# Kernel optimization log

Hardware: AMD Instinct MI355X
Metric: run time of the kernel (lower is better)

## Reference

```python
import jax, jax.numpy as jnp
import numpy as np

FEATURE_DIM = 4
LOSS_WEIGHT = 1.0
DELTA_V = 0.5
DELTA_D = 1.5
NUM_LABELS = 8  # instance ids 0..7; 0 = background
B, H, W = 16, 640, 640


def _safe_norm(x, axis):
    # L2 norm with grad-safe sqrt (forward value exact: 0 when sum of squares is 0)
    sq = jnp.sum(x * x, axis=axis)
    pos = sq > 0
    return jnp.where(pos, jnp.sqrt(jnp.where(pos, sq, 1.0)), 0.0)


def _single_loss(emb, instance, kernel, training_mask):
    # emb: [H,W,C], instance: [H,W] int, kernel/training_mask: [H,W] float
    C = emb.shape[-1]
    L = NUM_LABELS
    tm = training_mask > 0.5
    kr = kernel > 0.5
    inst = jnp.where(tm, instance, 0).reshape(-1)          # [P]
    inst_k = jnp.where(kr.reshape(-1), inst, 0)            # [P]
    emb_f = emb.reshape(-1, C)                              # [P,C]

    # per-label kernel-region means (emb_mean), label 0 column is zeros
    sums = jax.ops.segment_sum(emb_f, inst_k, num_segments=L)                       # [L,C]
    cnts = jax.ops.segment_sum(jnp.ones(inst_k.shape, jnp.float32), inst_k, L)      # [L]
    mu = sums / jnp.maximum(cnts, 1.0)[:, None]
    mu = mu.at[0].set(0.0)

    # aggregation term: per-pixel distance to its instance mean
    d = _safe_norm(emb_f - mu[inst], axis=1)                                         # [P]
    term = jnp.log(jnp.maximum(d - DELTA_V, 0.0) ** 2 + 1.0)
    cnt_i = jax.ops.segment_sum(jnp.ones(inst.shape, jnp.float32), inst, L)
    agg = jax.ops.segment_sum(term, inst, L) / jnp.maximum(cnt_i, 1.0)               # [L]
    # original skips label 0, then takes mean of l_agg[1:] -> drops first nonzero label
    l_agg = jnp.mean(agg[2:])

    # discrimination term: all ordered pairs of distinct nonzero labels
    dd = _safe_norm(mu[:, None, :] - mu[None, :, :], axis=-1)                        # [L,L]
    valid = (1.0 - jnp.eye(L, dtype=jnp.float32)).at[0, :].set(0.0).at[:, 0].set(0.0)
    dis = jnp.log(jnp.maximum(2.0 * DELTA_D - dd, 0.0) ** 2 + 1.0)
    l_dis = jnp.sum(dis * valid) / jnp.sum(valid)

    l_reg = jnp.mean(jnp.log(_safe_norm(mu, axis=1) + 1.0)) * 0.001
    return l_agg + l_dis + l_reg


def reference(emb, instance, kernel, training_mask):
    losses = jax.vmap(_single_loss)(emb, instance, kernel, training_mask)  # [B]
    return LOSS_WEIGHT * jnp.mean(losses)


def setup_inputs() -> dict:
    key = jax.random.key(0)
    k1, k2, k3 = jax.random.split(key, 3)
    emb = jax.random.normal(k1, (B, H, W, FEATURE_DIM), dtype=jnp.float32)
    instance = jax.random.randint(k2, (B, H, W), 0, NUM_LABELS, dtype=jnp.int32)
    kernel = jax.random.uniform(k3, (B, H, W), dtype=jnp.float32)
    training_mask = jnp.ones((B, H, W), dtype=jnp.float32)
    return {"emb": emb, "instance": instance, "kernel": kernel, "training_mask": training_mask}
```

## Files before the change

kernel.cpp:

```cpp
#include <hip/hip_runtime.h>
#include <math.h>

#define NLAB 8
#define BATCH 16
#define S_OFF  0
#define CK_OFF 28
#define CI_OFF 35
#define AG_OFF 41
#define ACC_PER_B 48
#define CNT_IDX (BATCH * ACC_PER_B)
#define ACC_ZERO_BYTES ((CNT_IDX + 1) * 4)
#define LAB_OFFSET 4096
#define GRID_X 64

__device__ __forceinline__ float wave_reduce(float v) {
#pragma unroll
  for (int off = 32; off > 0; off >>= 1) v += __shfl_xor(v, off, 64);
  return v;
}

__global__ __launch_bounds__(256, 4) void k_accum(
    const float4* __restrict__ emb, const int* __restrict__ inst,
    const float* __restrict__ ker, const float* __restrict__ tmk,
    float* __restrict__ acc, unsigned char* __restrict__ labc,
    int P, int use_cache)
{
  const int b = blockIdx.y;
  const size_t base = (size_t)b * P;
  const float4* e  = emb + base;
  const int*    ip = inst + base;
  const float*  kp = ker + base;
  const float*  tp = tmk + base;
  unsigned char* lb = labc + base;

  float s[28];
#pragma unroll
  for (int k = 0; k < 28; ++k) s[k] = 0.f;
  int ck[7] = {0, 0, 0, 0, 0, 0, 0};
  int ci[6] = {0, 0, 0, 0, 0, 0};

  const int lane = threadIdx.x & 63;
  const int wid  = threadIdx.x >> 6;
  const int ntiles = P >> 10;

  for (int t = blockIdx.x; t < ntiles; t += gridDim.x) {
    const int p0 = (t << 10) + (wid << 8) + lane;
    float4 e0 = e[p0];
    float4 e1 = e[p0 + 64];
    float4 e2 = e[p0 + 128];
    float4 e3 = e[p0 + 192];
    int   v0 = ip[p0], v1 = ip[p0 + 64], v2 = ip[p0 + 128], v3 = ip[p0 + 192];
    float q0 = kp[p0], q1 = kp[p0 + 64], q2 = kp[p0 + 128], q3 = kp[p0 + 192];
    float u0 = tp[p0], u1 = tp[p0 + 64], u2 = tp[p0 + 128], u3 = tp[p0 + 192];

    int lab0 = (u0 > 0.5f) ? (v0 & 7) : 0;
    int lab1 = (u1 > 0.5f) ? (v1 & 7) : 0;
    int lab2 = (u2 > 0.5f) ? (v2 & 7) : 0;
    int lab3 = (u3 > 0.5f) ? (v3 & 7) : 0;
    if (use_cache) {
      lb[p0]       = (unsigned char)lab0;
      lb[p0 + 64]  = (unsigned char)lab1;
      lb[p0 + 128] = (unsigned char)lab2;
      lb[p0 + 192] = (unsigned char)lab3;
    }
    int lk0 = (q0 > 0.5f) ? lab0 : 8;
    int lk1 = (q1 > 0.5f) ? lab1 : 8;
    int lk2 = (q2 > 0.5f) ? lab2 : 8;
    int lk3 = (q3 > 0.5f) ? lab3 : 8;

#pragma unroll
    for (int l = 1; l < NLAB; ++l) {
      bool h0 = (lk0 == l), h1 = (lk1 == l), h2 = (lk2 == l), h3 = (lk3 == l);
      ck[l - 1] += __popcll(__ballot(h0)) + __popcll(__ballot(h1)) +
                   __popcll(__ballot(h2)) + __popcll(__ballot(h3));
      float m0 = h0 ? 1.f : 0.f, m1 = h1 ? 1.f : 0.f;
      float m2 = h2 ? 1.f : 0.f, m3 = h3 ? 1.f : 0.f;
      const int o = (l - 1) * 4;
      s[o + 0] = fmaf(m0, e0.x, fmaf(m1, e1.x, fmaf(m2, e2.x, fmaf(m3, e3.x, s[o + 0]))));
      s[o + 1] = fmaf(m0, e0.y, fmaf(m1, e1.y, fmaf(m2, e2.y, fmaf(m3, e3.y, s[o + 1]))));
      s[o + 2] = fmaf(m0, e0.z, fmaf(m1, e1.z, fmaf(m2, e2.z, fmaf(m3, e3.z, s[o + 2]))));
      s[o + 3] = fmaf(m0, e0.w, fmaf(m1, e1.w, fmaf(m2, e2.w, fmaf(m3, e3.w, s[o + 3]))));
    }
#pragma unroll
    for (int l = 2; l < NLAB; ++l) {
      ci[l - 2] += __popcll(__ballot(lab0 == l)) + __popcll(__ballot(lab1 == l)) +
                   __popcll(__ballot(lab2 == l)) + __popcll(__ballot(lab3 == l));
    }
  }

  if (blockIdx.x == 0) {
    for (int p = (ntiles << 10) + (int)threadIdx.x; p < P; p += (int)blockDim.x) {
      int lab = (tp[p] > 0.5f) ? (ip[p] & 7) : 0;
      float kr = kp[p];
      float4 ev = e[p];
      if (lab >= 1 && kr > 0.5f) {
        atomicAdd(&acc[b * ACC_PER_B + (lab - 1) * 4 + 0], ev.x);
        atomicAdd(&acc[b * ACC_PER_B + (lab - 1) * 4 + 1], ev.y);
        atomicAdd(&acc[b * ACC_PER_B + (lab - 1) * 4 + 2], ev.z);
        atomicAdd(&acc[b * ACC_PER_B + (lab - 1) * 4 + 3], ev.w);
        atomicAdd(&acc[b * ACC_PER_B + CK_OFF + lab - 1], 1.f);
      }
      if (lab >= 2) atomicAdd(&acc[b * ACC_PER_B + CI_OFF + lab - 2], 1.f);
    }
  }

#pragma unroll
  for (int off = 32; off > 0; off >>= 1) {
    float tsh[28];
#pragma unroll
    for (int k = 0; k < 28; ++k) tsh[k] = __shfl_xor(s[k], off, 64);
#pragma unroll
    for (int k = 0; k < 28; ++k) s[k] += tsh[k];
  }

  __shared__ float redf[4][28];
  __shared__ int   redi[4][13];
  if (lane == 0) {
#pragma unroll
    for (int k = 0; k < 28; ++k) redf[wid][k] = s[k];
#pragma unroll
    for (int k = 0; k < 7; ++k) redi[wid][k] = ck[k];
#pragma unroll
    for (int k = 0; k < 6; ++k) redi[wid][7 + k] = ci[k];
  }
  __syncthreads();
  if (threadIdx.x < 28) {
    float v = redf[0][threadIdx.x] + redf[1][threadIdx.x] +
              redf[2][threadIdx.x] + redf[3][threadIdx.x];
    atomicAdd(acc + b * ACC_PER_B + S_OFF + threadIdx.x, v);
  } else if (threadIdx.x >= 32 && threadIdx.x < 32 + 13) {
    int j = threadIdx.x - 32;
    int v = redi[0][j] + redi[1][j] + redi[2][j] + redi[3][j];
    atomicAdd(acc + b * ACC_PER_B + CK_OFF + j, (float)v);
  }
}

__global__ __launch_bounds__(256, 4) void k_agg(
    const float4* __restrict__ emb, const int* __restrict__ inst,
    const float* __restrict__ tmk, const unsigned char* __restrict__ labc,
    float* __restrict__ acc, float* __restrict__ out,
    int P, int use_cache, int nblocks)
{
  const int b = blockIdx.y;
  const size_t base = (size_t)b * P;
  __shared__ float4 smu[NLAB];
  const float* accB = acc + b * ACC_PER_B;
  if (threadIdx.x < NLAB) {
    int l = threadIdx.x;
    float4 m = make_float4(0.f, 0.f, 0.f, 0.f);
    if (l > 0) {
      float inv = 1.f / fmaxf(accB[CK_OFF + l - 1], 1.f);
      m = make_float4(accB[S_OFF + (l - 1) * 4 + 0] * inv,
                      accB[S_OFF + (l - 1) * 4 + 1] * inv,
                      accB[S_OFF + (l - 1) * 4 + 2] * inv,
                      accB[S_OFF + (l - 1) * 4 + 3] * inv);
    }
    smu[l] = m;
  }
  __syncthreads();

  const float4* e = emb + base;
  const int*    ip = inst + base;
  const float*  tp = tmk + base;
  const unsigned char* lb = labc + base;

  float ag[6] = {0.f, 0.f, 0.f, 0.f, 0.f, 0.f};
  const int lane = threadIdx.x & 63;
  const int wid  = threadIdx.x >> 6;
  const int ntiles = P >> 10;

  for (int t = blockIdx.x; t < ntiles; t += gridDim.x) {
    const int p0 = (t << 10) + (wid << 8) + lane;
    int lab0, lab1, lab2, lab3;
    if (use_cache) {
      lab0 = lb[p0]; lab1 = lb[p0 + 64]; lab2 = lb[p0 + 128]; lab3 = lb[p0 + 192];
    } else {
      lab0 = (tp[p0] > 0.5f)       ? (ip[p0] & 7)       : 0;
      lab1 = (tp[p0 + 64] > 0.5f)  ? (ip[p0 + 64] & 7)  : 0;
      lab2 = (tp[p0 + 128] > 0.5f) ? (ip[p0 + 128] & 7) : 0;
      lab3 = (tp[p0 + 192] > 0.5f) ? (ip[p0 + 192] & 7) : 0;
    }
    float4 e0 = e[p0];
    float4 e1 = e[p0 + 64];
    float4 e2 = e[p0 + 128];
    float4 e3 = e[p0 + 192];

#pragma unroll
    for (int i = 0; i < 4; ++i) {
      int lab = (i == 0) ? lab0 : (i == 1) ? lab1 : (i == 2) ? lab2 : lab3;
      float4 ev = (i == 0) ? e0 : (i == 1) ? e1 : (i == 2) ? e2 : e3;
      float4 mv = smu[lab];
      float dx = ev.x - mv.x, dy = ev.y - mv.y;
      float dz = ev.z - mv.z, dw = ev.w - mv.w;
      float sq = dx * dx + dy * dy + dz * dz + dw * dw;
      float d = sqrtf(sq);
      float tt = fmaxf(d - 0.5f, 0.f);
      float term = logf(fmaf(tt, tt, 1.f));
#pragma unroll
      for (int l = 0; l < 6; ++l) ag[l] += (lab == l + 2) ? term : 0.f;
    }
  }

  if (blockIdx.x == 0) {
    for (int p = (ntiles << 10) + (int)threadIdx.x; p < P; p += (int)blockDim.x) {
      int lab = (tp[p] > 0.5f) ? (ip[p] & 7) : 0;
      if (lab >= 2) {
        float4 ev = e[p]; float4 mv = smu[lab];
        float dx = ev.x - mv.x, dy = ev.y - mv.y;
        float dz = ev.z - mv.z, dw = ev.w - mv.w;
        float d = sqrtf(dx * dx + dy * dy + dz * dz + dw * dw);
        float tt = fmaxf(d - 0.5f, 0.f);
        atomicAdd(&acc[b * ACC_PER_B + AG_OFF + lab - 2], logf(fmaf(tt, tt, 1.f)));
      }
    }
  }

#pragma unroll
  for (int off = 32; off > 0; off >>= 1) {
    float tsh[6];
#pragma unroll
    for (int k = 0; k < 6; ++k) tsh[k] = __shfl_xor(ag[k], off, 64);
#pragma unroll
    for (int k = 0; k < 6; ++k) ag[k] += tsh[k];
  }
  __shared__ float redf[4][6];
  if (lane == 0) {
#pragma unroll
    for (int k = 0; k < 6; ++k) redf[wid][k] = ag[k];
  }
  __syncthreads();
  if (threadIdx.x < 6) {
    float v = redf[0][threadIdx.x] + redf[1][threadIdx.x] +
              redf[2][threadIdx.x] + redf[3][threadIdx.x];
    atomicAdd(acc + b * ACC_PER_B + AG_OFF + threadIdx.x, v);
  }

  __syncthreads();
  __shared__ int amlast;
  if (threadIdx.x == 0) {
    __threadfence();
    unsigned int* cnt = (unsigned int*)(acc + CNT_IDX);
    unsigned int old = atomicAdd(cnt, 1u);
    amlast = (old == (unsigned int)(nblocks - 1)) ? 1 : 0;
  }
  __syncthreads();
  if (amlast && threadIdx.x < 64) {
    __threadfence();
    float loss = 0.f;
    if (threadIdx.x < BATCH) {
      const float* a = acc + threadIdx.x * ACC_PER_B;
      float av[47];
#pragma unroll
      for (int k = 0; k < 47; ++k)
        av[k] = __hip_atomic_load(&a[k], __ATOMIC_RELAXED, __HIP_MEMORY_SCOPE_AGENT);
      float mu[NLAB][4];
#pragma unroll
      for (int c = 0; c < 4; ++c) mu[0][c] = 0.f;
#pragma unroll
      for (int l = 1; l < NLAB; ++l) {
        float inv = 1.f / fmaxf(av[CK_OFF + l - 1], 1.f);
#pragma unroll
        for (int c = 0; c < 4; ++c) mu[l][c] = av[S_OFF + (l - 1) * 4 + c] * inv;
      }
      float l_agg = 0.f;
#pragma unroll
      for (int l = 2; l < NLAB; ++l)
        l_agg += av[AG_OFF + l - 2] / fmaxf(av[CI_OFF + l - 2], 1.f);
      l_agg *= (1.f / 6.f);
      float ssum = 0.f;
      for (int i = 1; i < NLAB; ++i)
        for (int j = 1; j < NLAB; ++j) {
          if (i == j) continue;
          float dx = mu[i][0] - mu[j][0], dy = mu[i][1] - mu[j][1];
          float dz = mu[i][2] - mu[j][2], dw = mu[i][3] - mu[j][3];
          float dd = sqrtf(dx * dx + dy * dy + dz * dz + dw * dw);
          float tt = fmaxf(3.0f - dd, 0.f);
          ssum += logf(fmaf(tt, tt, 1.f));
        }
      float l_dis = ssum / 42.f;
      float rsum = 0.f;
#pragma unroll
      for (int l = 1; l < NLAB; ++l) {
        float n = sqrtf(mu[l][0] * mu[l][0] + mu[l][1] * mu[l][1] +
                        mu[l][2] * mu[l][2] + mu[l][3] * mu[l][3]);
        rsum += logf(n + 1.f);
      }
      float l_reg = rsum * (0.001f / NLAB);
      loss = l_agg + l_dis + l_reg;
    }
    loss = wave_reduce(loss);
    if (threadIdx.x == 0) out[0] = loss * (1.f / BATCH);
  }
}

extern "C" void kernel_launch(void* const* d_in, const int* in_sizes, int n_in,
                              void* d_out, int out_size, void* d_ws, size_t ws_size,
                              hipStream_t stream) {
  const float4* emb  = (const float4*)d_in[0];
  const int*    inst = (const int*)d_in[1];
  const float*  ker  = (const float*)d_in[2];
  const float*  tmk  = (const float*)d_in[3];
  float* out = (float*)d_out;

  const int total = in_sizes[1];
  const int P = total / BATCH;

  float* acc = (float*)d_ws;
  unsigned char* labc = (unsigned char*)d_ws + LAB_OFFSET;
  const size_t need = (size_t)LAB_OFFSET + (size_t)total;
  const int use_cache = (ws_size >= need) ? 1 : 0;

  hipMemsetAsync(d_ws, 0, ACC_ZERO_BYTES, stream);

  dim3 grid(GRID_X, BATCH);
  k_accum<<<grid, 256, 0, stream>>>(emb, inst, ker, tmk, acc, labc, P, use_cache);
  k_agg  <<<grid, 256, 0, stream>>>(emb, inst, tmk, labc, acc, out, P, use_cache,
                                    GRID_X * BATCH);
}
```

Measured before the change: 272.3 us.

## Fuse accumulate and aggregate passes into one kernel with a grid barrier

```diff
diff --git a/kernel.cpp b/kernel.cpp
--- a/kernel.cpp
+++ b/kernel.cpp
@@ -8,10 +8,11 @@
 #define CI_OFF 35
 #define AG_OFF 41
 #define ACC_PER_B 48
-#define CNT_IDX (BATCH * ACC_PER_B)
-#define ACC_ZERO_BYTES ((CNT_IDX + 1) * 4)
-#define LAB_OFFSET 4096
-#define GRID_X 64
+#define CNT1_IDX (BATCH * ACC_PER_B)
+#define CNT2_IDX (BATCH * ACC_PER_B + 1)
+#define ACC_ZERO_BYTES ((BATCH * ACC_PER_B + 2) * 4)
+#define GX 64
+#define MAXK 8
 
 __device__ __forceinline__ float wave_reduce(float v) {
 #pragma unroll
@@ -19,19 +20,30 @@
   return v;
 }
 
-__global__ __launch_bounds__(256, 4) void k_accum(
+__global__ __launch_bounds__(256, 4) void k_fused(
     const float4* __restrict__ emb, const int* __restrict__ inst,
     const float* __restrict__ ker, const float* __restrict__ tmk,
-    float* __restrict__ acc, unsigned char* __restrict__ labc,
-    int P, int use_cache)
+    float* __restrict__ acc, float* __restrict__ out,
+    int P, int nblocks)
 {
+  __shared__ unsigned char labL[MAXK * 1024];
+  __shared__ float redf[4][28];
+  __shared__ int   redi[4][13];
+  __shared__ float accL[ACC_PER_B];
+  __shared__ float4 smu_s[NLAB];
+  __shared__ float redg[4][6];
+
   const int b = blockIdx.y;
   const size_t base = (size_t)b * P;
   const float4* e  = emb + base;
   const int*    ip = inst + base;
   const float*  kp = ker + base;
   const float*  tp = tmk + base;
-  unsigned char* lb = labc + base;
+
+  const int lane = threadIdx.x & 63;
+  const int wid  = threadIdx.x >> 6;
+  const int ntiles = P >> 10;
+  const int tail = P - (ntiles << 10);
 
   float s[28];
 #pragma unroll
@@ -39,56 +51,56 @@
   int ck[7] = {0, 0, 0, 0, 0, 0, 0};
   int ci[6] = {0, 0, 0, 0, 0, 0};
 
-  const int lane = threadIdx.x & 63;
-  const int wid  = threadIdx.x >> 6;
-  const int ntiles = P >> 10;
-
-  for (int t = blockIdx.x; t < ntiles; t += gridDim.x) {
-    const int p0 = (t << 10) + (wid << 8) + lane;
-    float4 e0 = e[p0];
-    float4 e1 = e[p0 + 64];
-    float4 e2 = e[p0 + 128];
-    float4 e3 = e[p0 + 192];
-    int   v0 = ip[p0], v1 = ip[p0 + 64], v2 = ip[p0 + 128], v3 = ip[p0 + 192];
-    float q0 = kp[p0], q1 = kp[p0 + 64], q2 = kp[p0 + 128], q3 = kp[p0 + 192];
-    float u0 = tp[p0], u1 = tp[p0 + 64], u2 = tp[p0 + 128], u3 = tp[p0 + 192];
-
-    int lab0 = (u0 > 0.5f) ? (v0 & 7) : 0;
-    int lab1 = (u1 > 0.5f) ? (v1 & 7) : 0;
-    int lab2 = (u2 > 0.5f) ? (v2 & 7) : 0;
-    int lab3 = (u3 > 0.5f) ? (v3 & 7) : 0;
-    if (use_cache) {
-      lb[p0]       = (unsigned char)lab0;
-      lb[p0 + 64]  = (unsigned char)lab1;
-      lb[p0 + 128] = (unsigned char)lab2;
-      lb[p0 + 192] = (unsigned char)lab3;
-    }
-    int lk0 = (q0 > 0.5f) ? lab0 : 8;
-    int lk1 = (q1 > 0.5f) ? lab1 : 8;
-    int lk2 = (q2 > 0.5f) ? lab2 : 8;
-    int lk3 = (q3 > 0.5f) ? lab3 : 8;
-
-#pragma unroll
-    for (int l = 1; l < NLAB; ++l) {
-      bool h0 = (lk0 == l), h1 = (lk1 == l), h2 = (lk2 == l), h3 = (lk3 == l);
-      ck[l - 1] += __popcll(__ballot(h0)) + __popcll(__ballot(h1)) +
-                   __popcll(__ballot(h2)) + __popcll(__ballot(h3));
-      float m0 = h0 ? 1.f : 0.f, m1 = h1 ? 1.f : 0.f;
-      float m2 = h2 ? 1.f : 0.f, m3 = h3 ? 1.f : 0.f;
-      const int o = (l - 1) * 4;
-      s[o + 0] = fmaf(m0, e0.x, fmaf(m1, e1.x, fmaf(m2, e2.x, fmaf(m3, e3.x, s[o + 0]))));
-      s[o + 1] = fmaf(m0, e0.y, fmaf(m1, e1.y, fmaf(m2, e2.y, fmaf(m3, e3.y, s[o + 1]))));
-      s[o + 2] = fmaf(m0, e0.z, fmaf(m1, e1.z, fmaf(m2, e2.z, fmaf(m3, e3.z, s[o + 2]))));
-      s[o + 3] = fmaf(m0, e0.w, fmaf(m1, e1.w, fmaf(m2, e2.w, fmaf(m3, e3.w, s[o + 3]))));
-    }
-#pragma unroll
-    for (int l = 2; l < NLAB; ++l) {
-      ci[l - 2] += __popcll(__ballot(lab0 == l)) + __popcll(__ballot(lab1 == l)) +
-                   __popcll(__ballot(lab2 == l)) + __popcll(__ballot(lab3 == l));
-    }
-  }
-
-  if (blockIdx.x == 0) {
+  {
+    int k = 0;
+    for (int t = blockIdx.x; t < ntiles; t += GX, ++k) {
+      const int p0 = (t << 10) + (wid << 8) + lane;
+      float4 e0 = e[p0];
+      float4 e1 = e[p0 + 64];
+      float4 e2 = e[p0 + 128];
+      float4 e3 = e[p0 + 192];
+      int   v0 = ip[p0], v1 = ip[p0 + 64], v2 = ip[p0 + 128], v3 = ip[p0 + 192];
+      float q0 = kp[p0], q1 = kp[p0 + 64], q2 = kp[p0 + 128], q3 = kp[p0 + 192];
+      float u0 = tp[p0], u1 = tp[p0 + 64], u2 = tp[p0 + 128], u3 = tp[p0 + 192];
+
+      int lab0 = (u0 > 0.5f) ? (v0 & 7) : 0;
+      int lab1 = (u1 > 0.5f) ? (v1 & 7) : 0;
+      int lab2 = (u2 > 0.5f) ? (v2 & 7) : 0;
+      int lab3 = (u3 > 0.5f) ? (v3 & 7) : 0;
+      if (k < MAXK) {
+        const int lo = (k << 10) + (wid << 8) + lane;
+        labL[lo]       = (unsigned char)lab0;
+        labL[lo + 64]  = (unsigned char)lab1;
+        labL[lo + 128] = (unsigned char)lab2;
+        labL[lo + 192] = (unsigned char)lab3;
+      }
+      int lk0 = (q0 > 0.5f) ? lab0 : 8;
+      int lk1 = (q1 > 0.5f) ? lab1 : 8;
+      int lk2 = (q2 > 0.5f) ? lab2 : 8;
+      int lk3 = (q3 > 0.5f) ? lab3 : 8;
+
+#pragma unroll
+      for (int l = 1; l < NLAB; ++l) {
+        bool h0 = (lk0 == l), h1 = (lk1 == l), h2 = (lk2 == l), h3 = (lk3 == l);
+        ck[l - 1] += __popcll(__ballot(h0)) + __popcll(__ballot(h1)) +
+                     __popcll(__ballot(h2)) + __popcll(__ballot(h3));
+        float m0 = h0 ? 1.f : 0.f, m1 = h1 ? 1.f : 0.f;
+        float m2 = h2 ? 1.f : 0.f, m3 = h3 ? 1.f : 0.f;
+        const int o = (l - 1) * 4;
+        s[o + 0] = fmaf(m0, e0.x, fmaf(m1, e1.x, fmaf(m2, e2.x, fmaf(m3, e3.x, s[o + 0]))));
+        s[o + 1] = fmaf(m0, e0.y, fmaf(m1, e1.y, fmaf(m2, e2.y, fmaf(m3, e3.y, s[o + 1]))));
+        s[o + 2] = fmaf(m0, e0.z, fmaf(m1, e1.z, fmaf(m2, e2.z, fmaf(m3, e3.z, s[o + 2]))));
+        s[o + 3] = fmaf(m0, e0.w, fmaf(m1, e1.w, fmaf(m2, e2.w, fmaf(m3, e3.w, s[o + 3]))));
+      }
+#pragma unroll
+      for (int l = 2; l < NLAB; ++l) {
+        ci[l - 2] += __popcll(__ballot(lab0 == l)) + __popcll(__ballot(lab1 == l)) +
+                     __popcll(__ballot(lab2 == l)) + __popcll(__ballot(lab3 == l));
+      }
+    }
+  }
+
+  if (tail && blockIdx.x == 0) {
     for (int p = (ntiles << 10) + (int)threadIdx.x; p < P; p += (int)blockDim.x) {
       int lab = (tp[p] > 0.5f) ? (ip[p] & 7) : 0;
       float kr = kp[p];
@@ -102,6 +114,7 @@
       }
       if (lab >= 2) atomicAdd(&acc[b * ACC_PER_B + CI_OFF + lab - 2], 1.f);
     }
+    __threadfence();
   }
 
 #pragma unroll
@@ -112,9 +125,6 @@
 #pragma unroll
     for (int k = 0; k < 28; ++k) s[k] += tsh[k];
   }
-
-  __shared__ float redf[4][28];
-  __shared__ int   redi[4][13];
   if (lane == 0) {
 #pragma unroll
     for (int k = 0; k < 28; ++k) redf[wid][k] = s[k];
@@ -133,75 +143,75 @@
     int v = redi[0][j] + redi[1][j] + redi[2][j] + redi[3][j];
     atomicAdd(acc + b * ACC_PER_B + CK_OFF + j, (float)v);
   }
-}
-
-__global__ __launch_bounds__(256, 4) void k_agg(
-    const float4* __restrict__ emb, const int* __restrict__ inst,
-    const float* __restrict__ tmk, const unsigned char* __restrict__ labc,
-    float* __restrict__ acc, float* __restrict__ out,
-    int P, int use_cache, int nblocks)
-{
-  const int b = blockIdx.y;
-  const size_t base = (size_t)b * P;
-  __shared__ float4 smu[NLAB];
-  const float* accB = acc + b * ACC_PER_B;
+
+  if (threadIdx.x == 0) {
+    unsigned int* cnt = (unsigned int*)(acc + CNT1_IDX);
+    __hip_atomic_fetch_add(cnt, 1u, __ATOMIC_ACQ_REL, __HIP_MEMORY_SCOPE_AGENT);
+    while (__hip_atomic_load(cnt, __ATOMIC_ACQUIRE, __HIP_MEMORY_SCOPE_AGENT)
+           < (unsigned int)nblocks)
+      __builtin_amdgcn_s_sleep(2);
+  }
+  __syncthreads();
+
+  if (threadIdx.x < 47)
+    accL[threadIdx.x] = __hip_atomic_load(&acc[b * ACC_PER_B + threadIdx.x],
+                                          __ATOMIC_RELAXED, __HIP_MEMORY_SCOPE_AGENT);
+  __syncthreads();
   if (threadIdx.x < NLAB) {
     int l = threadIdx.x;
     float4 m = make_float4(0.f, 0.f, 0.f, 0.f);
     if (l > 0) {
-      float inv = 1.f / fmaxf(accB[CK_OFF + l - 1], 1.f);
-      m = make_float4(accB[S_OFF + (l - 1) * 4 + 0] * inv,
-                      accB[S_OFF + (l - 1) * 4 + 1] * inv,
-                      accB[S_OFF + (l - 1) * 4 + 2] * inv,
-                      accB[S_OFF + (l - 1) * 4 + 3] * inv);
-    }
-    smu[l] = m;
-  }
-  __syncthreads();
-
-  const float4* e = emb + base;
-  const int*    ip = inst + base;
-  const float*  tp = tmk + base;
-  const unsigned char* lb = labc + base;
+      float inv = 1.f / fmaxf(accL[CK_OFF + l - 1], 1.f);
+      m = make_float4(accL[S_OFF + (l - 1) * 4 + 0] * inv,
+                      accL[S_OFF + (l - 1) * 4 + 1] * inv,
+                      accL[S_OFF + (l - 1) * 4 + 2] * inv,
+                      accL[S_OFF + (l - 1) * 4 + 3] * inv);
+    }
+    smu_s[l] = m;
+  }
+  __syncthreads();
+  float4 smu[NLAB];
+#pragma unroll
+  for (int l = 0; l < NLAB; ++l) smu[l] = smu_s[l];
 
   float ag[6] = {0.f, 0.f, 0.f, 0.f, 0.f, 0.f};
-  const int lane = threadIdx.x & 63;
-  const int wid  = threadIdx.x >> 6;
-  const int ntiles = P >> 10;
-
-  for (int t = blockIdx.x; t < ntiles; t += gridDim.x) {
-    const int p0 = (t << 10) + (wid << 8) + lane;
-    int lab0, lab1, lab2, lab3;
-    if (use_cache) {
-      lab0 = lb[p0]; lab1 = lb[p0 + 64]; lab2 = lb[p0 + 128]; lab3 = lb[p0 + 192];
-    } else {
-      lab0 = (tp[p0] > 0.5f)       ? (ip[p0] & 7)       : 0;
-      lab1 = (tp[p0 + 64] > 0.5f)  ? (ip[p0 + 64] & 7)  : 0;
-      lab2 = (tp[p0 + 128] > 0.5f) ? (ip[p0 + 128] & 7) : 0;
-      lab3 = (tp[p0 + 192] > 0.5f) ? (ip[p0 + 192] & 7) : 0;
-    }
-    float4 e0 = e[p0];
-    float4 e1 = e[p0 + 64];
-    float4 e2 = e[p0 + 128];
-    float4 e3 = e[p0 + 192];
-
-#pragma unroll
-    for (int i = 0; i < 4; ++i) {
-      int lab = (i == 0) ? lab0 : (i == 1) ? lab1 : (i == 2) ? lab2 : lab3;
-      float4 ev = (i == 0) ? e0 : (i == 1) ? e1 : (i == 2) ? e2 : e3;
-      float4 mv = smu[lab];
-      float dx = ev.x - mv.x, dy = ev.y - mv.y;
-      float dz = ev.z - mv.z, dw = ev.w - mv.w;
-      float sq = dx * dx + dy * dy + dz * dz + dw * dw;
-      float d = sqrtf(sq);
-      float tt = fmaxf(d - 0.5f, 0.f);
-      float term = logf(fmaf(tt, tt, 1.f));
-#pragma unroll
-      for (int l = 0; l < 6; ++l) ag[l] += (lab == l + 2) ? term : 0.f;
-    }
-  }
-
-  if (blockIdx.x == 0) {
+  {
+    int k = 0;
+    for (int t = blockIdx.x; t < ntiles; t += GX, ++k) {
+      const int p0 = (t << 10) + (wid << 8) + lane;
+      int lab0, lab1, lab2, lab3;
+      if (k < MAXK) {
+        const int lo = (k << 10) + (wid << 8) + lane;
+        lab0 = labL[lo]; lab1 = labL[lo + 64];
+        lab2 = labL[lo + 128]; lab3 = labL[lo + 192];
+      } else {
+        lab0 = (tp[p0] > 0.5f)       ? (ip[p0] & 7)       : 0;
+        lab1 = (tp[p0 + 64] > 0.5f)  ? (ip[p0 + 64] & 7)  : 0;
+        lab2 = (tp[p0 + 128] > 0.5f) ? (ip[p0 + 128] & 7) : 0;
+        lab3 = (tp[p0 + 192] > 0.5f) ? (ip[p0 + 192] & 7) : 0;
+      }
+      float4 e0 = e[p0];
+      float4 e1 = e[p0 + 64];
+      float4 e2 = e[p0 + 128];
+      float4 e3 = e[p0 + 192];
+
+#pragma unroll
+      for (int i = 0; i < 4; ++i) {
+        int lab = (i == 0) ? lab0 : (i == 1) ? lab1 : (i == 2) ? lab2 : lab3;
+        float4 ev = (i == 0) ? e0 : (i == 1) ? e1 : (i == 2) ? e2 : e3;
+        float4 mv = smu[lab];
+        float dx = ev.x - mv.x, dy = ev.y - mv.y;
+        float dz = ev.z - mv.z, dw = ev.w - mv.w;
+        float d = sqrtf(dx * dx + dy * dy + dz * dz + dw * dw);
+        float tt = fmaxf(d - 0.5f, 0.f);
+        float term = logf(fmaf(tt, tt, 1.f));
+#pragma unroll
+        for (int l = 0; l < 6; ++l) ag[l] += (lab == l + 2) ? term : 0.f;
+      }
+    }
+  }
+
+  if (tail && blockIdx.x == 0) {
     for (int p = (ntiles << 10) + (int)threadIdx.x; p < P; p += (int)blockDim.x) {
       int lab = (tp[p] > 0.5f) ? (ip[p] & 7) : 0;
       if (lab >= 2) {
@@ -213,6 +223,7 @@
         atomicAdd(&acc[b * ACC_PER_B + AG_OFF + lab - 2], logf(fmaf(tt, tt, 1.f)));
       }
     }
+    __threadfence();
   }
 
 #pragma unroll
@@ -223,29 +234,27 @@
 #pragma unroll
     for (int k = 0; k < 6; ++k) ag[k] += tsh[k];
   }
-  __shared__ float redf[4][6];
   if (lane == 0) {
 #pragma unroll
-    for (int k = 0; k < 6; ++k) redf[wid][k] = ag[k];
+    for (int k = 0; k < 6; ++k) redg[wid][k] = ag[k];
   }
   __syncthreads();
   if (threadIdx.x < 6) {
-    float v = redf[0][threadIdx.x] + redf[1][threadIdx.x] +
-              redf[2][threadIdx.x] + redf[3][threadIdx.x];
+    float v = redg[0][threadIdx.x] + redg[1][threadIdx.x] +
+              redg[2][threadIdx.x] + redg[3][threadIdx.x];
     atomicAdd(acc + b * ACC_PER_B + AG_OFF + threadIdx.x, v);
   }
 
   __syncthreads();
   __shared__ int amlast;
   if (threadIdx.x == 0) {
-    __threadfence();
-    unsigned int* cnt = (unsigned int*)(acc + CNT_IDX);
-    unsigned int old = atomicAdd(cnt, 1u);
+    unsigned int* cnt = (unsigned int*)(acc + CNT2_IDX);
+    unsigned int old = __hip_atomic_fetch_add(cnt, 1u, __ATOMIC_ACQ_REL,
+                                              __HIP_MEMORY_SCOPE_AGENT);
     amlast = (old == (unsigned int)(nblocks - 1)) ? 1 : 0;
   }
   __syncthreads();
   if (amlast && threadIdx.x < 64) {
-    __threadfence();
     float loss = 0.f;
     if (threadIdx.x < BATCH) {
       const float* a = acc + threadIdx.x * ACC_PER_B;
@@ -306,14 +315,9 @@
   const int P = total / BATCH;
 
   float* acc = (float*)d_ws;
-  unsigned char* labc = (unsigned char*)d_ws + LAB_OFFSET;
-  const size_t need = (size_t)LAB_OFFSET + (size_t)total;
-  const int use_cache = (ws_size >= need) ? 1 : 0;
 
   hipMemsetAsync(d_ws, 0, ACC_ZERO_BYTES, stream);
 
-  dim3 grid(GRID_X, BATCH);
-  k_accum<<<grid, 256, 0, stream>>>(emb, inst, ker, tmk, acc, labc, P, use_cache);
-  k_agg  <<<grid, 256, 0, stream>>>(emb, inst, tmk, labc, acc, out, P, use_cache,
-                                    GRID_X * BATCH);
+  dim3 grid(GX, BATCH);
+  k_fused<<<grid, 256, 0, stream>>>(emb, inst, ker, tmk, acc, out, P, GX * BATCH);
 }
```

Measured after the change: 444.5 us. 63.2% more time.

## Process 16 contiguous pixels per thread with vectorized loads and packed label cache

Applied to the files above, without the earlier changes.

```diff
diff --git a/kernel.cpp b/kernel.cpp
--- a/kernel.cpp
+++ b/kernel.cpp
@@ -11,7 +11,11 @@
 #define CNT_IDX (BATCH * ACC_PER_B)
 #define ACC_ZERO_BYTES ((CNT_IDX + 1) * 4)
 #define LAB_OFFSET 4096
-#define GRID_X 64
+#define GX 64
+
+#define GETI(v, c) ((c) == 0 ? (v).x : (c) == 1 ? (v).y : (c) == 2 ? (v).z : (v).w)
+#define GETF(v, c) ((c) == 0 ? (v).x : (c) == 1 ? (v).y : (c) == 2 ? (v).z : (v).w)
+#define GETU(v, c) ((c) == 0 ? (v).x : (c) == 1 ? (v).y : (c) == 2 ? (v).z : (v).w)
 
 __device__ __forceinline__ float wave_reduce(float v) {
 #pragma unroll
@@ -19,11 +23,11 @@
   return v;
 }
 
-__global__ __launch_bounds__(256, 4) void k_accum(
+__global__ __launch_bounds__(256, 2) void k_accum(
     const float4* __restrict__ emb, const int* __restrict__ inst,
     const float* __restrict__ ker, const float* __restrict__ tmk,
     float* __restrict__ acc, unsigned char* __restrict__ labc,
-    int P, int use_cache)
+    int P, int use_cache, int fast)
 {
   const int b = blockIdx.y;
   const size_t base = (size_t)b * P;
@@ -39,60 +43,74 @@
   int ck[7] = {0, 0, 0, 0, 0, 0, 0};
   int ci[6] = {0, 0, 0, 0, 0, 0};
 
-  const int lane = threadIdx.x & 63;
-  const int wid  = threadIdx.x >> 6;
-  const int ntiles = P >> 10;
-
-  for (int t = blockIdx.x; t < ntiles; t += gridDim.x) {
-    const int p0 = (t << 10) + (wid << 8) + lane;
-    float4 e0 = e[p0];
-    float4 e1 = e[p0 + 64];
-    float4 e2 = e[p0 + 128];
-    float4 e3 = e[p0 + 192];
-    int   v0 = ip[p0], v1 = ip[p0 + 64], v2 = ip[p0 + 128], v3 = ip[p0 + 192];
-    float q0 = kp[p0], q1 = kp[p0 + 64], q2 = kp[p0 + 128], q3 = kp[p0 + 192];
-    float u0 = tp[p0], u1 = tp[p0 + 64], u2 = tp[p0 + 128], u3 = tp[p0 + 192];
-
-    int lab0 = (u0 > 0.5f) ? (v0 & 7) : 0;
-    int lab1 = (u1 > 0.5f) ? (v1 & 7) : 0;
-    int lab2 = (u2 > 0.5f) ? (v2 & 7) : 0;
-    int lab3 = (u3 > 0.5f) ? (v3 & 7) : 0;
-    if (use_cache) {
-      lb[p0]       = (unsigned char)lab0;
-      lb[p0 + 64]  = (unsigned char)lab1;
-      lb[p0 + 128] = (unsigned char)lab2;
-      lb[p0 + 192] = (unsigned char)lab3;
-    }
-    int lk0 = (q0 > 0.5f) ? lab0 : 8;
-    int lk1 = (q1 > 0.5f) ? lab1 : 8;
-    int lk2 = (q2 > 0.5f) ? lab2 : 8;
-    int lk3 = (q3 > 0.5f) ? lab3 : 8;
-
-#pragma unroll
-    for (int l = 1; l < NLAB; ++l) {
-      bool h0 = (lk0 == l), h1 = (lk1 == l), h2 = (lk2 == l), h3 = (lk3 == l);
-      ck[l - 1] += __popcll(__ballot(h0)) + __popcll(__ballot(h1)) +
-                   __popcll(__ballot(h2)) + __popcll(__ballot(h3));
-      float m0 = h0 ? 1.f : 0.f, m1 = h1 ? 1.f : 0.f;
-      float m2 = h2 ? 1.f : 0.f, m3 = h3 ? 1.f : 0.f;
-      const int o = (l - 1) * 4;
-      s[o + 0] = fmaf(m0, e0.x, fmaf(m1, e1.x, fmaf(m2, e2.x, fmaf(m3, e3.x, s[o + 0]))));
-      s[o + 1] = fmaf(m0, e0.y, fmaf(m1, e1.y, fmaf(m2, e2.y, fmaf(m3, e3.y, s[o + 1]))));
-      s[o + 2] = fmaf(m0, e0.z, fmaf(m1, e1.z, fmaf(m2, e2.z, fmaf(m3, e3.z, s[o + 2]))));
-      s[o + 3] = fmaf(m0, e0.w, fmaf(m1, e1.w, fmaf(m2, e2.w, fmaf(m3, e3.w, s[o + 3]))));
-    }
-#pragma unroll
-    for (int l = 2; l < NLAB; ++l) {
-      ci[l - 2] += __popcll(__ballot(lab0 == l)) + __popcll(__ballot(lab1 == l)) +
-                   __popcll(__ballot(lab2 == l)) + __popcll(__ballot(lab3 == l));
-    }
-  }
-
-  if (blockIdx.x == 0) {
-    for (int p = (ntiles << 10) + (int)threadIdx.x; p < P; p += (int)blockDim.x) {
+  const int tid = blockIdx.x * blockDim.x + threadIdx.x;
+  const int nthreads = gridDim.x * blockDim.x;
+
+  if (fast) {
+    const int nu = P >> 4;
+    const int4*   ip4 = (const int4*)ip;
+    const float4* kp4 = (const float4*)kp;
+    const float4* tp4 = (const float4*)tp;
+    uint4* lb4 = (uint4*)lb;
+
+    for (int u = tid; u < nu; u += nthreads) {
+      int4   iv[4]; float4 kv[4], tv[4]; float4 ev[16];
+#pragma unroll
+      for (int a = 0; a < 4; ++a) iv[a] = ip4[u * 4 + a];
+#pragma unroll
+      for (int a = 0; a < 4; ++a) kv[a] = kp4[u * 4 + a];
+#pragma unroll
+      for (int a = 0; a < 4; ++a) tv[a] = tp4[u * 4 + a];
+#pragma unroll
+      for (int j = 0; j < 16; ++j) ev[j] = e[u * 16 + j];
+
+      int lab[16], lk[16];
+#pragma unroll
+      for (int j = 0; j < 16; ++j) {
+        int   v = GETI(iv[j >> 2], j & 3);
+        float q = GETF(kv[j >> 2], j & 3);
+        float t = GETF(tv[j >> 2], j & 3);
+        lab[j] = (t > 0.5f) ? (v & 7) : 0;
+        lk[j]  = (q > 0.5f) ? lab[j] : 8;
+      }
+      if (use_cache) {
+        uint4 pk;
+        pk.x = (unsigned)lab[0]  | ((unsigned)lab[1]  << 8) | ((unsigned)lab[2]  << 16) | ((unsigned)lab[3]  << 24);
+        pk.y = (unsigned)lab[4]  | ((unsigned)lab[5]  << 8) | ((unsigned)lab[6]  << 16) | ((unsigned)lab[7]  << 24);
+        pk.z = (unsigned)lab[8]  | ((unsigned)lab[9]  << 8) | ((unsigned)lab[10] << 16) | ((unsigned)lab[11] << 24);
+        pk.w = (unsigned)lab[12] | ((unsigned)lab[13] << 8) | ((unsigned)lab[14] << 16) | ((unsigned)lab[15] << 24);
+        lb4[u] = pk;
+      }
+#pragma unroll
+      for (int l = 1; l < NLAB; ++l) {
+        int c = 0;
+        const int o = (l - 1) * 4;
+#pragma unroll
+        for (int j = 0; j < 16; ++j) {
+          bool h = (lk[j] == l);
+          c += __popcll(__ballot(h));
+          float m = h ? 1.f : 0.f;
+          s[o + 0] = fmaf(m, ev[j].x, s[o + 0]);
+          s[o + 1] = fmaf(m, ev[j].y, s[o + 1]);
+          s[o + 2] = fmaf(m, ev[j].z, s[o + 2]);
+          s[o + 3] = fmaf(m, ev[j].w, s[o + 3]);
+        }
+        ck[l - 1] += c;
+      }
+#pragma unroll
+      for (int l = 2; l < NLAB; ++l) {
+        int c = 0;
+#pragma unroll
+        for (int j = 0; j < 16; ++j) c += __popcll(__ballot(lab[j] == l));
+        ci[l - 2] += c;
+      }
+    }
+    const int p0 = nu << 4;
+    for (int p = p0 + tid; p < P; p += nthreads) {
       int lab = (tp[p] > 0.5f) ? (ip[p] & 7) : 0;
       float kr = kp[p];
       float4 ev = e[p];
+      if (use_cache) lb[p] = (unsigned char)lab;
       if (lab >= 1 && kr > 0.5f) {
         atomicAdd(&acc[b * ACC_PER_B + (lab - 1) * 4 + 0], ev.x);
         atomicAdd(&acc[b * ACC_PER_B + (lab - 1) * 4 + 1], ev.y);
@@ -102,8 +120,25 @@
       }
       if (lab >= 2) atomicAdd(&acc[b * ACC_PER_B + CI_OFF + lab - 2], 1.f);
     }
-  }
-
+  } else {
+    for (int p = tid; p < P; p += nthreads) {
+      int lab = (tp[p] > 0.5f) ? (ip[p] & 7) : 0;
+      float kr = kp[p];
+      float4 ev = e[p];
+      if (use_cache) lb[p] = (unsigned char)lab;
+      if (lab >= 1 && kr > 0.5f) {
+        atomicAdd(&acc[b * ACC_PER_B + (lab - 1) * 4 + 0], ev.x);
+        atomicAdd(&acc[b * ACC_PER_B + (lab - 1) * 4 + 1], ev.y);
+        atomicAdd(&acc[b * ACC_PER_B + (lab - 1) * 4 + 2], ev.z);
+        atomicAdd(&acc[b * ACC_PER_B + (lab - 1) * 4 + 3], ev.w);
+        atomicAdd(&acc[b * ACC_PER_B + CK_OFF + lab - 1], 1.f);
+      }
+      if (lab >= 2) atomicAdd(&acc[b * ACC_PER_B + CI_OFF + lab - 2], 1.f);
+    }
+  }
+
+  const int lane = threadIdx.x & 63;
+  const int wid  = threadIdx.x >> 6;
 #pragma unroll
   for (int off = 32; off > 0; off >>= 1) {
     float tsh[28];
@@ -112,7 +147,6 @@
 #pragma unroll
     for (int k = 0; k < 28; ++k) s[k] += tsh[k];
   }
-
   __shared__ float redf[4][28];
   __shared__ int   redi[4][13];
   if (lane == 0) {
@@ -135,15 +169,15 @@
   }
 }
 
-__global__ __launch_bounds__(256, 4) void k_agg(
+__global__ __launch_bounds__(256, 2) void k_agg(
     const float4* __restrict__ emb, const int* __restrict__ inst,
     const float* __restrict__ tmk, const unsigned char* __restrict__ labc,
     float* __restrict__ acc, float* __restrict__ out,
-    int P, int use_cache, int nblocks)
+    int P, int use_cache, int fast, int nblocks)
 {
   const int b = blockIdx.y;
   const size_t base = (size_t)b * P;
-  __shared__ float4 smu[NLAB];
+  __shared__ float4 smu_s[NLAB];
   const float* accB = acc + b * ACC_PER_B;
   if (threadIdx.x < NLAB) {
     int l = threadIdx.x;
@@ -155,54 +189,65 @@
                       accB[S_OFF + (l - 1) * 4 + 2] * inv,
                       accB[S_OFF + (l - 1) * 4 + 3] * inv);
     }
-    smu[l] = m;
-  }
-  __syncthreads();
-
-  const float4* e = emb + base;
+    smu_s[l] = m;
+  }
+  __syncthreads();
+  float4 smu[NLAB];
+#pragma unroll
+  for (int l = 0; l < NLAB; ++l) smu[l] = smu_s[l];
+
+  const float4* e  = emb + base;
   const int*    ip = inst + base;
   const float*  tp = tmk + base;
   const unsigned char* lb = labc + base;
 
   float ag[6] = {0.f, 0.f, 0.f, 0.f, 0.f, 0.f};
-  const int lane = threadIdx.x & 63;
-  const int wid  = threadIdx.x >> 6;
-  const int ntiles = P >> 10;
-
-  for (int t = blockIdx.x; t < ntiles; t += gridDim.x) {
-    const int p0 = (t << 10) + (wid << 8) + lane;
-    int lab0, lab1, lab2, lab3;
-    if (use_cache) {
-      lab0 = lb[p0]; lab1 = lb[p0 + 64]; lab2 = lb[p0 + 128]; lab3 = lb[p0 + 192];
-    } else {
-      lab0 = (tp[p0] > 0.5f)       ? (ip[p0] & 7)       : 0;
-      lab1 = (tp[p0 + 64] > 0.5f)  ? (ip[p0 + 64] & 7)  : 0;
-      lab2 = (tp[p0 + 128] > 0.5f) ? (ip[p0 + 128] & 7) : 0;
-      lab3 = (tp[p0 + 192] > 0.5f) ? (ip[p0 + 192] & 7) : 0;
-    }
-    float4 e0 = e[p0];
-    float4 e1 = e[p0 + 64];
-    float4 e2 = e[p0 + 128];
-    float4 e3 = e[p0 + 192];
-
-#pragma unroll
-    for (int i = 0; i < 4; ++i) {
-      int lab = (i == 0) ? lab0 : (i == 1) ? lab1 : (i == 2) ? lab2 : lab3;
-      float4 ev = (i == 0) ? e0 : (i == 1) ? e1 : (i == 2) ? e2 : e3;
-      float4 mv = smu[lab];
-      float dx = ev.x - mv.x, dy = ev.y - mv.y;
-      float dz = ev.z - mv.z, dw = ev.w - mv.w;
-      float sq = dx * dx + dy * dy + dz * dz + dw * dw;
-      float d = sqrtf(sq);
-      float tt = fmaxf(d - 0.5f, 0.f);
-      float term = logf(fmaf(tt, tt, 1.f));
-#pragma unroll
-      for (int l = 0; l < 6; ++l) ag[l] += (lab == l + 2) ? term : 0.f;
-    }
-  }
-
-  if (blockIdx.x == 0) {
-    for (int p = (ntiles << 10) + (int)threadIdx.x; p < P; p += (int)blockDim.x) {
+  const int tid = blockIdx.x * blockDim.x + threadIdx.x;
+  const int nthreads = gridDim.x * blockDim.x;
+
+  if (fast) {
+    const int nu = P >> 4;
+    const uint4* lb4 = (const uint4*)lb;
+    const int4*   ip4 = (const int4*)ip;
+    const float4* tp4 = (const float4*)tp;
+
+    for (int u = tid; u < nu; u += nthreads) {
+      float4 ev[16];
+#pragma unroll
+      for (int j = 0; j < 16; ++j) ev[j] = e[u * 16 + j];
+      int lab[16];
+      if (use_cache) {
+        uint4 lq = lb4[u];
+#pragma unroll
+        for (int j = 0; j < 16; ++j)
+          lab[j] = (GETU(lq, j >> 2) >> ((j & 3) * 8)) & 7;
+      } else {
+        int4 iv[4]; float4 tv[4];
+#pragma unroll
+        for (int a = 0; a < 4; ++a) iv[a] = ip4[u * 4 + a];
+#pragma unroll
+        for (int a = 0; a < 4; ++a) tv[a] = tp4[u * 4 + a];
+#pragma unroll
+        for (int j = 0; j < 16; ++j) {
+          int   v = GETI(iv[j >> 2], j & 3);
+          float t = GETF(tv[j >> 2], j & 3);
+          lab[j] = (t > 0.5f) ? (v & 7) : 0;
+        }
+      }
+#pragma unroll
+      for (int j = 0; j < 16; ++j) {
+        float4 mv = smu[lab[j]];
+        float dx = ev[j].x - mv.x, dy = ev[j].y - mv.y;
+        float dz = ev[j].z - mv.z, dw = ev[j].w - mv.w;
+        float d = sqrtf(dx * dx + dy * dy + dz * dz + dw * dw);
+        float tt = fmaxf(d - 0.5f, 0.f);
+        float term = logf(fmaf(tt, tt, 1.f));
+#pragma unroll
+        for (int l = 0; l < 6; ++l) ag[l] += (lab[j] == l + 2) ? term : 0.f;
+      }
+    }
+    const int p0 = nu << 4;
+    for (int p = p0 + tid; p < P; p += nthreads) {
       int lab = (tp[p] > 0.5f) ? (ip[p] & 7) : 0;
       if (lab >= 2) {
         float4 ev = e[p]; float4 mv = smu[lab];
@@ -213,8 +258,22 @@
         atomicAdd(&acc[b * ACC_PER_B + AG_OFF + lab - 2], logf(fmaf(tt, tt, 1.f)));
       }
     }
-  }
-
+  } else {
+    for (int p = tid; p < P; p += nthreads) {
+      int lab = (tp[p] > 0.5f) ? (ip[p] & 7) : 0;
+      if (lab >= 2) {
+        float4 ev = e[p]; float4 mv = smu[lab];
+        float dx = ev.x - mv.x, dy = ev.y - mv.y;
+        float dz = ev.z - mv.z, dw = ev.w - mv.w;
+        float d = sqrtf(dx * dx + dy * dy + dz * dz + dw * dw);
+        float tt = fmaxf(d - 0.5f, 0.f);
+        atomicAdd(&acc[b * ACC_PER_B + AG_OFF + lab - 2], logf(fmaf(tt, tt, 1.f)));
+      }
+    }
+  }
+
+  const int lane = threadIdx.x & 63;
+  const int wid  = threadIdx.x >> 6;
 #pragma unroll
   for (int off = 32; off > 0; off >>= 1) {
     float tsh[6];
@@ -223,29 +282,28 @@
 #pragma unroll
     for (int k = 0; k < 6; ++k) ag[k] += tsh[k];
   }
-  __shared__ float redf[4][6];
+  __shared__ float redg[4][6];
   if (lane == 0) {
 #pragma unroll
-    for (int k = 0; k < 6; ++k) redf[wid][k] = ag[k];
+    for (int k = 0; k < 6; ++k) redg[wid][k] = ag[k];
   }
   __syncthreads();
   if (threadIdx.x < 6) {
-    float v = redf[0][threadIdx.x] + redf[1][threadIdx.x] +
-              redf[2][threadIdx.x] + redf[3][threadIdx.x];
+    float v = redg[0][threadIdx.x] + redg[1][threadIdx.x] +
+              redg[2][threadIdx.x] + redg[3][threadIdx.x];
     atomicAdd(acc + b * ACC_PER_B + AG_OFF + threadIdx.x, v);
   }
 
   __syncthreads();
   __shared__ int amlast;
   if (threadIdx.x == 0) {
-    __threadfence();
     unsigned int* cnt = (unsigned int*)(acc + CNT_IDX);
-    unsigned int old = atomicAdd(cnt, 1u);
+    unsigned int old = __hip_atomic_fetch_add(cnt, 1u, __ATOMIC_ACQ_REL,
+                                              __HIP_MEMORY_SCOPE_AGENT);
     amlast = (old == (unsigned int)(nblocks - 1)) ? 1 : 0;
   }
   __syncthreads();
   if (amlast && threadIdx.x < 64) {
-    __threadfence();
     float loss = 0.f;
     if (threadIdx.x < BATCH) {
       const float* a = acc + threadIdx.x * ACC_PER_B;
@@ -309,11 +367,13 @@
   unsigned char* labc = (unsigned char*)d_ws + LAB_OFFSET;
   const size_t need = (size_t)LAB_OFFSET + (size_t)total;
   const int use_cache = (ws_size >= need) ? 1 : 0;
+  const int fast = ((P & 15) == 0) ? 1 : 0;
 
   hipMemsetAsync(d_ws, 0, ACC_ZERO_BYTES, stream);
 
-  dim3 grid(GRID_X, BATCH);
-  k_accum<<<grid, 256, 0, stream>>>(emb, inst, ker, tmk, acc, labc, P, use_cache);
-  k_agg  <<<grid, 256, 0, stream>>>(emb, inst, tmk, labc, acc, out, P, use_cache,
-                                    GRID_X * BATCH);
+  dim3 grid(GX, BATCH);
+  k_accum<<<grid, 256, 0, stream>>>(emb, inst, ker, tmk, acc, labc, P,
+                                    use_cache, fast);
+  k_agg  <<<grid, 256, 0, stream>>>(emb, inst, tmk, labc, acc, out, P,
+                                    use_cache, fast, GX * BATCH);
 }
```

Result: slower. 313.9 us (+15.3%).
